# Kernel tuning notes

Hardware: AMD Instinct MI355X
Metric: run time of the kernel (lower is better)

Reference implementation:

```python
import jax, jax.numpy as jnp
import numpy as np

B = 32768   # batch (agents)
H = 64      # h_dim
E = 16      # embedding_dim
M = 6       # num_modes (n_samples)
P = M * 2   # traj_points
T = 30      # pred_len (seq_len)


def setup_inputs() -> dict:
    key = jax.random.key(0)
    ks = jax.random.split(key, 14)
    def s(k, shape, scale=0.1):
        return jax.random.normal(k, shape, jnp.float32) * scale
    return dict(
        traj_abs=s(ks[0], (1, B, 2), 1.0),
        traj_rel=s(ks[1], (1, B, 2), 1.0),
        h0=s(ks[2], (1, B, H)),
        c0=s(ks[3], (1, B, H)),
        W_ih=s(ks[4], (4 * H, E)),
        W_hh=s(ks[5], (4 * H, H)),
        b_ih=s(ks[6], (4 * H,)),
        b_hh=s(ks[7], (4 * H,)),
        W_se=s(ks[8], (E, P)),
        b_se=s(ks[9], (E,)),
        W_pos=s(ks[10], (P, H)),
        b_pos=s(ks[11], (P,)),
        W_conf=s(ks[12], (M, H)),
        b_conf=s(ks[13], (M,)),
    )


def reference(traj_abs, traj_rel, h0, c0, W_ih, W_hh, b_ih, b_hh,
              W_se, b_se, W_pos, b_pos, W_conf, b_conf):
    b = traj_rel.shape[1]
    # repeat_interleave the (x,y) pair num_modes times along feature dim -> [b, 12]
    rel12 = jnp.tile(traj_rel.reshape(b, 1, 2), (1, M, 1)).reshape(b, P)
    x = jax.nn.leaky_relu(rel12 @ W_se.T + b_se)  # [b, E]
    h = h0[0]
    c = c0[0]

    def step(carry, _):
        x, h, c = carry
        # PyTorch LSTM cell, gate order i, f, g, o
        gates = x @ W_ih.T + b_ih + h @ W_hh.T + b_hh  # [b, 4H]
        i, f, g, o = jnp.split(gates, 4, axis=-1)
        c = jax.nn.sigmoid(f) * c + jax.nn.sigmoid(i) * jnp.tanh(g)
        h = jax.nn.sigmoid(o) * jnp.tanh(c)
        rel = h @ W_pos.T + b_pos                      # [b, P]
        x = jax.nn.leaky_relu(rel @ W_se.T + b_se)     # [b, E]
        return (x, h, c), rel

    (x, h, c), rels = jax.lax.scan(step, (x, h, c), None, length=T)  # rels: [T, b, P]
    pred = rels.reshape(T, b, M, 2).transpose(1, 2, 0, 3)            # [b, M, T, 2]
    conf = jax.nn.softmax(h @ W_conf.T + b_conf, axis=1)             # [b, M]
    return pred, conf
```

## Files before the change

kernel.cpp:

```cpp
#include <hip/hip_runtime.h>
#include <hip/hip_bf16.h>

typedef _Float16 half8 __attribute__((ext_vector_type(8)));
typedef _Float16 half4 __attribute__((ext_vector_type(4)));
typedef float floatx16 __attribute__((ext_vector_type(16)));
typedef float float4v __attribute__((ext_vector_type(4)));

#define BATCH 32768
#define TT 30

#if __has_builtin(__builtin_amdgcn_exp2f)
#define FEXP2(x) __builtin_amdgcn_exp2f(x)
#else
#define FEXP2(x) __expf((x) * 0.6931471805599453f)
#endif
#if __has_builtin(__builtin_amdgcn_rcpf)
#define FRCP(x) __builtin_amdgcn_rcpf(x)
#else
#define FRCP(x) (1.0f / (x))
#endif

#define NLOG2E  -1.4426950408889634f
#define N2LOG2E -2.8853900817779268f

#define WFRAG_OFF 0
#define WCF_OFF   10240
#define BIASB_OFF 12288
#define SXY_OFF   12544
#define CBIAS_OFF 12592
#define WCONF_OFF 12656
#define BCONF_OFF 13040
#define FLAG_IDX  13056
#define CONF_BASE (BATCH * 360)

__global__ void detect_kernel(const unsigned short* __restrict__ raw,
                              int* __restrict__ flag_out) {
    __shared__ int sflag[256];
    int local = 0;
    for (int i = threadIdx.x; i < 16384; i += 256) {
        unsigned short u = raw[i];
        if ((u & 0x7F80u) == 0x7F80u) local = 1;
    }
    sflag[threadIdx.x] = local;
    __syncthreads();
    if (threadIdx.x == 0) {
        int f = 0;
        for (int i = 0; i < 256; ++i) f |= sflag[i];
        flag_out[0] = f;
    }
}

__device__ __forceinline__ float ldin(const void* p, int i, int isf32) {
    return isf32 ? ((const float*)p)[i]
                 : (float)((const __hip_bfloat16*)p)[i];
}

__global__ void prep_kernel(const void* __restrict__ W_ih,
                            const void* __restrict__ W_hh,
                            const void* __restrict__ b_ih,
                            const void* __restrict__ b_hh,
                            const void* __restrict__ W_se,
                            const void* __restrict__ b_se,
                            const void* __restrict__ W_pos,
                            const void* __restrict__ b_pos,
                            const void* __restrict__ W_conf,
                            const void* __restrict__ b_conf,
                            float* __restrict__ ws)
{
    const int isf32 = ((const int*)(ws + FLAG_IDX))[0];
    int tid = blockIdx.x * blockDim.x + threadIdx.x;
    int stride = gridDim.x * blockDim.x;
    _Float16* wfh = (_Float16*)ws;

    for (int idx = tid; idx < 20480; idx += stride) {
        int tl = idx / 2560, r1 = idx % 2560;
        int ks = r1 / 512, r2 = r1 % 512;
        int lane = r2 >> 3, jj = r2 & 7;
        int gate = tl >> 1, ug = tl & 1;
        int k = ks * 16 + (lane >> 5) * 8 + jj;
        int jn = ug * 32 + (lane & 31);
        int row = gate * 64 + jn;
        float v = (k < 16) ? ldin(W_ih, row * 16 + k, isf32)
                           : ldin(W_hh, row * 64 + (k - 16), isf32);
        v *= (gate == 2) ? N2LOG2E : NLOG2E;
        wfh[idx] = (_Float16)v;
    }
    _Float16* wch = (_Float16*)(ws + WCF_OFF);
    for (int idx = tid; idx < 4096; idx += stride) {
        int w = idx >> 11, r1 = idx & 2047;
        int ks = r1 >> 9, r2 = r1 & 511;
        int lane = r2 >> 3, jj = r2 & 7;
        int n = lane & 31;
        int krel = ks * 16 + (lane >> 5) * 8 + jj;
        float v = 0.f;
        if (w == 0) {
            if (n < 12) v = ldin(W_pos, n * 64 + krel, isf32);
        } else if (n < 16) {
            float s = 0.f;
            for (int p = 0; p < 12; ++p)
                s += ldin(W_se, n * 12 + p, isf32) * ldin(W_pos, p * 64 + krel, isf32);
            v = s;
        }
        wch[idx] = (_Float16)v;
    }
    for (int idx = tid; idx < 256; idx += stride) {
        int gate = idx >> 6;
        float scale = (gate == 2) ? N2LOG2E : NLOG2E;
        ws[BIASB_OFF + idx] = (ldin(b_ih, idx, isf32) + ldin(b_hh, idx, isf32)) * scale;
    }
    for (int idx = tid; idx < 16; idx += stride) {
        float sx = 0.f, sy = 0.f;
        for (int m = 0; m < 6; ++m) {
            sx += ldin(W_se, idx * 12 + 2 * m, isf32);
            sy += ldin(W_se, idx * 12 + 2 * m + 1, isf32);
        }
        ws[SXY_OFF + idx * 3 + 0] = sx;
        ws[SXY_OFF + idx * 3 + 1] = sy;
        ws[SXY_OFF + idx * 3 + 2] = ldin(b_se, idx, isf32);
    }
    for (int idx = tid; idx < 64; idx += stride) {
        int w = idx >> 5, cc = idx & 31;
        float v = 0.f;
        if (w == 0) {
            if (cc < 12) v = ldin(b_pos, cc, isf32);
        } else if (cc < 16) {
            float s = ldin(b_se, cc, isf32);
            for (int p = 0; p < 12; ++p)
                s += ldin(W_se, cc * 12 + p, isf32) * ldin(b_pos, p, isf32);
            v = s;
        }
        ws[CBIAS_OFF + idx] = v;
    }
    for (int idx = tid; idx < 384; idx += stride)
        ws[WCONF_OFF + idx] = ldin(W_conf, idx, isf32);
    for (int idx = tid; idx < 6; idx += stride)
        ws[BCONF_OFF + idx] = ldin(b_conf, idx, isf32);
}

__global__ __launch_bounds__(128, 2) void lstm_kernel(
    const void* __restrict__ traj_rel,
    const void* __restrict__ h0,
    const void* __restrict__ c0,
    const float* __restrict__ ws,
    float* __restrict__ out)
{
    __shared__ _Float16 zsh[32 * 88];
    __shared__ _Float16 predh[12 * 30 * 36];

    const int tid = threadIdx.x;
    const int lane = tid & 63;
    const int ug = __builtin_amdgcn_readfirstlane(tid >> 6);
    const int col = lane & 31;
    const int half = lane >> 5;
    const int j = ug * 32 + col;
    const int base = blockIdx.x * 32;
    const int isf32 = ((const int*)(ws + FLAG_IDX))[0];

    const float4v* wfg = (const float4v*)ws;
    half8 Bf[4][5];
#pragma unroll
    for (int g = 0; g < 4; ++g)
#pragma unroll
        for (int ks = 0; ks < 5; ++ks)
            Bf[g][ks] = __builtin_bit_cast(half8,
                wfg[((g * 2 + ug) * 5 + ks) * 64 + lane]);
    float bias4[4];
#pragma unroll
    for (int g = 0; g < 4; ++g) bias4[g] = ws[BIASB_OFF + g * 64 + j];

    half8 wfc[4];
    {
        const float4v* wcg = (const float4v*)(ws + WCF_OFF);
#pragma unroll
        for (int ks = 0; ks < 4; ++ks)
            wfc[ks] = __builtin_bit_cast(half8, wcg[(ug * 4 + ks) * 64 + lane]);
    }
    const float cb = ws[CBIAS_OFF + ug * 32 + col];

    float c[16];
#pragma unroll
    for (int i = 0; i < 16; ++i) {
        int r = (i & 3) + 8 * (i >> 2) + 4 * half;
        c[i] = ldin(c0, (base + r) * 64 + j, isf32);
    }
    {
        int m = tid & 31, jq = tid >> 5;
        half8 ha, hb;
#pragma unroll
        for (int i = 0; i < 8; ++i)
            ha[i] = (_Float16)ldin(h0, (base + m) * 64 + jq * 16 + i, isf32);
#pragma unroll
        for (int i = 0; i < 8; ++i)
            hb[i] = (_Float16)ldin(h0, (base + m) * 64 + jq * 16 + 8 + i, isf32);
        *(half8*)&zsh[m * 88 + 16 + jq * 16] = ha;
        *(half8*)&zsh[m * 88 + 16 + jq * 16 + 8] = hb;
        float rx = ldin(traj_rel, 2 * (base + m), isf32);
        float ry = ldin(traj_rel, 2 * (base + m) + 1, isf32);
        half4 xs;
#pragma unroll
        for (int i = 0; i < 4; ++i) {
            int e = 4 * jq + i;
            float x = fmaf(rx, ws[SXY_OFF + e * 3],
                      fmaf(ry, ws[SXY_OFF + e * 3 + 1], ws[SXY_OFF + e * 3 + 2]));
            xs[i] = (_Float16)(x > 0.f ? x : 0.01f * x);
        }
        *(half4*)&zsh[m * 88 + 4 * jq] = xs;
    }
    __syncthreads();

    const int zb = col * 88 + half * 8;

    for (int t = 0; t < TT; ++t) {
        floatx16 acc[4];
#pragma unroll
        for (int g = 0; g < 4; ++g)
#pragma unroll
            for (int i = 0; i < 16; ++i) acc[g][i] = bias4[g];
#pragma unroll
        for (int ks = 0; ks < 5; ++ks) {
            half8 af = *(const half8*)&zsh[zb + ks * 16];
#pragma unroll
            for (int g = 0; g < 4; ++g)
                acc[g] = __builtin_amdgcn_mfma_f32_32x32x16_f16(af, Bf[g][ks], acc[g], 0, 0, 0);
        }
        __syncthreads();

#pragma unroll
        for (int i = 0; i < 16; ++i) {
            float si = FRCP(1.0f + FEXP2(acc[0][i]));
            float sf = FRCP(1.0f + FEXP2(acc[1][i]));
            float tg = fmaf(2.0f, FRCP(1.0f + FEXP2(acc[2][i])), -1.0f);
            float so = FRCP(1.0f + FEXP2(acc[3][i]));
            float cn = fmaf(sf, c[i], si * tg);
            c[i] = cn;
            float th = fmaf(2.0f, FRCP(1.0f + FEXP2(cn * N2LOG2E)), -1.0f);
            float hn = so * th;
            int r = (i & 3) + 8 * (i >> 2) + 4 * half;
            zsh[r * 88 + 16 + j] = (_Float16)hn;
        }
        __syncthreads();

        {
            floatx16 racc;
#pragma unroll
            for (int i = 0; i < 16; ++i) racc[i] = cb;
#pragma unroll
            for (int ks = 0; ks < 4; ++ks) {
                half8 af = *(const half8*)&zsh[zb + 16 + ks * 16];
                racc = __builtin_amdgcn_mfma_f32_32x32x16_f16(af, wfc[ks], racc, 0, 0, 0);
            }
            if (ug == 0) {
                if (col < 12) {
#pragma unroll
                    for (int q2 = 0; q2 < 4; ++q2) {
                        half4 hv;
#pragma unroll
                        for (int i = 0; i < 4; ++i) hv[i] = (_Float16)racc[q2 * 4 + i];
                        *(half4*)&predh[(col * 30 + t) * 36 + q2 * 8 + 4 * half] = hv;
                    }
                }
            } else if (t != TT - 1) {
                if (col < 16) {
#pragma unroll
                    for (int i = 0; i < 16; ++i) {
                        float xv = racc[i];
                        xv = xv > 0.f ? xv : 0.01f * xv;
                        int r = (i & 3) + 8 * (i >> 2) + 4 * half;
                        zsh[r * 88 + col] = (_Float16)xv;
                    }
                }
            }
        }
        __syncthreads();
    }

    {
        float4* po4 = (float4*)(out + (size_t)base * 360);
#pragma unroll 1
        for (int q2 = 0; q2 < 23; ++q2) {
            int idx4 = q2 * 128 + tid;
            if (idx4 < 2880) {
                int a = idx4 / 90, rem = idx4 % 90;
                int m = rem / 15, tq = rem % 15;
                int t0 = tq * 2;
                float4 o;
                o.x = (float)predh[((2 * m + 0) * 30 + t0) * 36 + a];
                o.y = (float)predh[((2 * m + 1) * 30 + t0) * 36 + a];
                o.z = (float)predh[((2 * m + 0) * 30 + t0 + 1) * 36 + a];
                o.w = (float)predh[((2 * m + 1) * 30 + t0 + 1) * 36 + a];
                po4[idx4] = o;
            }
        }
    }

    if (ug == 0 && half == 0) {
        int m = col;
        float l[6];
#pragma unroll
        for (int md = 0; md < 6; ++md) l[md] = ws[BCONF_OFF + md];
        for (int jj = 0; jj < 64; ++jj) {
            float hv = (float)zsh[m * 88 + 16 + jj];
#pragma unroll
            for (int md = 0; md < 6; ++md)
                l[md] = fmaf(hv, ws[WCONF_OFF + md * 64 + jj], l[md]);
        }
        float mx = l[0];
#pragma unroll
        for (int md = 1; md < 6; ++md) mx = fmaxf(mx, l[md]);
        float ex[6], s = 0.f;
#pragma unroll
        for (int md = 0; md < 6; ++md) { ex[md] = __expf(l[md] - mx); s += ex[md]; }
        float inv = FRCP(s);
#pragma unroll
        for (int md = 0; md < 6; ++md)
            out[CONF_BASE + (size_t)(base + m) * 6 + md] = ex[md] * inv;
    }
}

extern "C" void kernel_launch(void* const* d_in, const int* in_sizes, int n_in,
                              void* d_out, int out_size, void* d_ws, size_t ws_size,
                              hipStream_t stream) {
    const void* traj_rel = d_in[1];
    const void* h0   = d_in[2];
    const void* c0   = d_in[3];
    const void* W_ih = d_in[4];
    const void* W_hh = d_in[5];
    const void* b_ih = d_in[6];
    const void* b_hh = d_in[7];
    const void* W_se = d_in[8];
    const void* b_se = d_in[9];
    const void* W_pos  = d_in[10];
    const void* b_pos  = d_in[11];
    const void* W_conf = d_in[12];
    const void* b_conf = d_in[13];
    float* ws = (float*)d_ws;
    float* out = (float*)d_out;

    detect_kernel<<<1, 256, 0, stream>>>((const unsigned short*)W_hh,
                                         (int*)(ws + FLAG_IDX));
    prep_kernel<<<40, 256, 0, stream>>>(W_ih, W_hh, b_ih, b_hh, W_se, b_se,
                                        W_pos, b_pos, W_conf, b_conf, ws);
    lstm_kernel<<<BATCH / 32, 128, 0, stream>>>(traj_rel, h0, c0, ws, out);
}
```

Baseline: 218.8 us.

## Split batch tile into two 16-row groups and software-pipeline LSTM phases

Switches the recurrent gate and projection matmuls from 32x32x16 to 16x16x32 MFMA, with weights re-laid out per wave over 32-unit halves. The 32-row tile is split into two 16-row groups so one group's gate matmul overlaps with the other group's activation math and output projection, giving three barriers per step that each cover two groups. The goal is to keep the matrix cores busy while the transcendental-heavy elementwise phase runs. The cost is padded K (80 to 96), more weight fragments held in registers, and more complex scheduling.

```diff
diff --git a/kernel.cpp b/kernel.cpp
--- a/kernel.cpp
+++ b/kernel.cpp
@@ -3,7 +3,6 @@
 
 typedef _Float16 half8 __attribute__((ext_vector_type(8)));
 typedef _Float16 half4 __attribute__((ext_vector_type(4)));
-typedef float floatx16 __attribute__((ext_vector_type(16)));
 typedef float float4v __attribute__((ext_vector_type(4)));
 
 #define BATCH 32768
@@ -24,13 +23,13 @@
 #define N2LOG2E -2.8853900817779268f
 
 #define WFRAG_OFF 0
-#define WCF_OFF   10240
-#define BIASB_OFF 12288
-#define SXY_OFF   12544
-#define CBIAS_OFF 12592
-#define WCONF_OFF 12656
-#define BCONF_OFF 13040
-#define FLAG_IDX  13056
+#define WCF_OFF   12288
+#define BIASB_OFF 13312
+#define SXY_OFF   13568
+#define CBIAS_OFF 13616
+#define WCONF_OFF 13648
+#define BCONF_OFF 14032
+#define FLAG_IDX  14038
 #define CONF_BASE (BATCH * 360)
 
 __global__ void detect_kernel(const unsigned short* __restrict__ raw,
@@ -72,33 +71,35 @@
     int stride = gridDim.x * blockDim.x;
     _Float16* wfh = (_Float16*)ws;
 
-    for (int idx = tid; idx < 20480; idx += stride) {
-        int tl = idx / 2560, r1 = idx % 2560;
-        int ks = r1 / 512, r2 = r1 % 512;
-        int lane = r2 >> 3, jj = r2 & 7;
-        int gate = tl >> 1, ug = tl & 1;
-        int k = ks * 16 + (lane >> 5) * 8 + jj;
-        int jn = ug * 32 + (lane & 31);
-        int row = gate * 64 + jn;
-        float v = (k < 16) ? ldin(W_ih, row * 16 + k, isf32)
-                           : ldin(W_hh, row * 64 + (k - 16), isf32);
+    for (int idx = tid; idx < 24576; idx += stride) {
+        int jj = idx & 7, r = idx >> 3;
+        int lane = r & 63; r >>= 6;
+        int ks = r % 3; r /= 3;
+        int tl = r & 7; int uhh = r >> 3;
+        int col = lane & 15, akq = lane >> 4;
+        int k = ks * 32 + akq * 8 + jj;
+        int gate = tl >> 1, us = tl & 1;
+        int row = gate * 64 + uhh * 32 + us * 16 + col;
+        float v = 0.f;
+        if (k < 16) v = ldin(W_ih, row * 16 + k, isf32);
+        else if (k < 80) v = ldin(W_hh, row * 64 + (k - 16), isf32);
         v *= (gate == 2) ? N2LOG2E : NLOG2E;
         wfh[idx] = (_Float16)v;
     }
     _Float16* wch = (_Float16*)(ws + WCF_OFF);
-    for (int idx = tid; idx < 4096; idx += stride) {
-        int w = idx >> 11, r1 = idx & 2047;
-        int ks = r1 >> 9, r2 = r1 & 511;
-        int lane = r2 >> 3, jj = r2 & 7;
-        int n = lane & 31;
-        int krel = ks * 16 + (lane >> 5) * 8 + jj;
+    for (int idx = tid; idx < 2048; idx += stride) {
+        int jj = idx & 7, r = idx >> 3;
+        int lane = r & 63; r >>= 6;
+        int ks = r & 1, uhh = r >> 1;
+        int col = lane & 15, akq = lane >> 4;
+        int k = ks * 32 + akq * 8 + jj;
         float v = 0.f;
-        if (w == 0) {
-            if (n < 12) v = ldin(W_pos, n * 64 + krel, isf32);
-        } else if (n < 16) {
+        if (uhh == 0) {
+            if (col < 12) v = ldin(W_pos, col * 64 + k, isf32);
+        } else {
             float s = 0.f;
             for (int p = 0; p < 12; ++p)
-                s += ldin(W_se, n * 12 + p, isf32) * ldin(W_pos, p * 64 + krel, isf32);
+                s += ldin(W_se, col * 12 + p, isf32) * ldin(W_pos, p * 64 + k, isf32);
             v = s;
         }
         wch[idx] = (_Float16)v;
@@ -118,12 +119,12 @@
         ws[SXY_OFF + idx * 3 + 1] = sy;
         ws[SXY_OFF + idx * 3 + 2] = ldin(b_se, idx, isf32);
     }
-    for (int idx = tid; idx < 64; idx += stride) {
-        int w = idx >> 5, cc = idx & 31;
+    for (int idx = tid; idx < 32; idx += stride) {
+        int w = idx >> 4, cc = idx & 15;
         float v = 0.f;
         if (w == 0) {
             if (cc < 12) v = ldin(b_pos, cc, isf32);
-        } else if (cc < 16) {
+        } else {
             float s = ldin(b_se, cc, isf32);
             for (int p = 0; p < 12; ++p)
                 s += ldin(W_se, cc * 12 + p, isf32) * ldin(b_pos, p, isf32);
@@ -144,47 +145,51 @@
     const float* __restrict__ ws,
     float* __restrict__ out)
 {
-    __shared__ _Float16 zsh[32 * 88];
+    __shared__ _Float16 zsh[2 * 16 * 104];
     __shared__ _Float16 predh[12 * 30 * 36];
 
     const int tid = threadIdx.x;
     const int lane = tid & 63;
-    const int ug = __builtin_amdgcn_readfirstlane(tid >> 6);
-    const int col = lane & 31;
-    const int half = lane >> 5;
-    const int j = ug * 32 + col;
+    const int uh = __builtin_amdgcn_readfirstlane(tid >> 6);
+    const int col16 = lane & 15;
+    const int akq = lane >> 4;
     const int base = blockIdx.x * 32;
     const int isf32 = ((const int*)(ws + FLAG_IDX))[0];
 
     const float4v* wfg = (const float4v*)ws;
-    half8 Bf[4][5];
-#pragma unroll
-    for (int g = 0; g < 4; ++g)
-#pragma unroll
-        for (int ks = 0; ks < 5; ++ks)
-            Bf[g][ks] = __builtin_bit_cast(half8,
-                wfg[((g * 2 + ug) * 5 + ks) * 64 + lane]);
-    float bias4[4];
-#pragma unroll
-    for (int g = 0; g < 4; ++g) bias4[g] = ws[BIASB_OFF + g * 64 + j];
-
-    half8 wfc[4];
+    half8 Bf[8][3];
+#pragma unroll
+    for (int tl = 0; tl < 8; ++tl)
+#pragma unroll
+        for (int ks = 0; ks < 3; ++ks)
+            Bf[tl][ks] = __builtin_bit_cast(half8,
+                wfg[((uh * 8 + tl) * 3 + ks) * 64 + lane]);
+    float bias8[8];
+#pragma unroll
+    for (int tl = 0; tl < 8; ++tl)
+        bias8[tl] = ws[BIASB_OFF + (tl >> 1) * 64 + uh * 32 + (tl & 1) * 16 + col16];
+    half8 wfc[2];
     {
         const float4v* wcg = (const float4v*)(ws + WCF_OFF);
 #pragma unroll
-        for (int ks = 0; ks < 4; ++ks)
-            wfc[ks] = __builtin_bit_cast(half8, wcg[(ug * 4 + ks) * 64 + lane]);
-    }
-    const float cb = ws[CBIAS_OFF + ug * 32 + col];
-
-    float c[16];
-#pragma unroll
-    for (int i = 0; i < 16; ++i) {
-        int r = (i & 3) + 8 * (i >> 2) + 4 * half;
-        c[i] = ldin(c0, (base + r) * 64 + j, isf32);
-    }
+        for (int ks = 0; ks < 2; ++ks)
+            wfc[ks] = __builtin_bit_cast(half8, wcg[(uh * 2 + ks) * 64 + lane]);
+    }
+    const float cb = ws[CBIAS_OFF + uh * 16 + col16];
+
+    float cg0[8], cg1[8];
+#pragma unroll
+    for (int us = 0; us < 2; ++us)
+#pragma unroll
+        for (int i = 0; i < 4; ++i) {
+            int unit = uh * 32 + us * 16 + col16;
+            cg0[us * 4 + i] = ldin(c0, (base + akq * 4 + i) * 64 + unit, isf32);
+            cg1[us * 4 + i] = ldin(c0, (base + 16 + akq * 4 + i) * 64 + unit, isf32);
+        }
     {
         int m = tid & 31, jq = tid >> 5;
+        int g = m >> 4, row = m & 15;
+        _Float16* zg = &zsh[g * 1664];
         half8 ha, hb;
 #pragma unroll
         for (int i = 0; i < 8; ++i)
@@ -192,8 +197,8 @@
 #pragma unroll
         for (int i = 0; i < 8; ++i)
             hb[i] = (_Float16)ldin(h0, (base + m) * 64 + jq * 16 + 8 + i, isf32);
-        *(half8*)&zsh[m * 88 + 16 + jq * 16] = ha;
-        *(half8*)&zsh[m * 88 + 16 + jq * 16 + 8] = hb;
+        *(half8*)&zg[row * 104 + 16 + jq * 16] = ha;
+        *(half8*)&zg[row * 104 + 16 + jq * 16 + 8] = hb;
         float rx = ldin(traj_rel, 2 * (base + m), isf32);
         float ry = ldin(traj_rel, 2 * (base + m) + 1, isf32);
         half4 xs;
@@ -204,75 +209,104 @@
                       fmaf(ry, ws[SXY_OFF + e * 3 + 1], ws[SXY_OFF + e * 3 + 2]));
             xs[i] = (_Float16)(x > 0.f ? x : 0.01f * x);
         }
-        *(half4*)&zsh[m * 88 + 4 * jq] = xs;
-    }
-    __syncthreads();
-
-    const int zb = col * 88 + half * 8;
-
-    for (int t = 0; t < TT; ++t) {
-        floatx16 acc[4];
-#pragma unroll
-        for (int g = 0; g < 4; ++g)
-#pragma unroll
-            for (int i = 0; i < 16; ++i) acc[g][i] = bias4[g];
-#pragma unroll
-        for (int ks = 0; ks < 5; ++ks) {
-            half8 af = *(const half8*)&zsh[zb + ks * 16];
-#pragma unroll
-            for (int g = 0; g < 4; ++g)
-                acc[g] = __builtin_amdgcn_mfma_f32_32x32x16_f16(af, Bf[g][ks], acc[g], 0, 0, 0);
-        }
+        *(half4*)&zg[row * 104 + 4 * jq] = xs;
+        if (jq == 0) {
+            half8 zz = {};
+            *(half8*)&zg[row * 104 + 80] = zz;
+            *(half8*)&zg[row * 104 + 88] = zz;
+        }
+    }
+    __syncthreads();
+
+    const int zbA = col16 * 104 + akq * 8;
+    const int zbC = zbA + 16;
+    const int hwb = 16 + uh * 32 + col16;
+
+    float4v acc0[8], acc1[8];
+
+#define ZG(g) (&zsh[(g) * 1664])
+
+#define PHASE_A(G, ACC) do {                                                  \
+    _Float16* zg_ = ZG(G);                                                    \
+    _Pragma("unroll")                                                         \
+    for (int tl = 0; tl < 8; ++tl) {                                          \
+        float bv = bias8[tl];                                                 \
+        ACC[tl][0] = bv; ACC[tl][1] = bv; ACC[tl][2] = bv; ACC[tl][3] = bv;   \
+    }                                                                         \
+    _Pragma("unroll")                                                         \
+    for (int ks = 0; ks < 3; ++ks) {                                          \
+        half8 af_ = *(const half8*)&zg_[zbA + ks * 32];                       \
+        _Pragma("unroll")                                                     \
+        for (int tl = 0; tl < 8; ++tl)                                        \
+            ACC[tl] = __builtin_amdgcn_mfma_f32_16x16x32_f16(                 \
+                af_, Bf[tl][ks], ACC[tl], 0, 0, 0);                           \
+    }                                                                         \
+} while (0)
+
+#define PHASE_B(G, ACC, CARR) do {                                            \
+    _Float16* zg_ = ZG(G);                                                    \
+    _Pragma("unroll")                                                         \
+    for (int us = 0; us < 2; ++us) {                                          \
+        _Pragma("unroll")                                                     \
+        for (int i = 0; i < 4; ++i) {                                         \
+            float si = FRCP(1.0f + FEXP2(ACC[us][i]));                        \
+            float sf = FRCP(1.0f + FEXP2(ACC[2 + us][i]));                    \
+            float tg = fmaf(2.0f, FRCP(1.0f + FEXP2(ACC[4 + us][i])), -1.0f); \
+            float so = FRCP(1.0f + FEXP2(ACC[6 + us][i]));                    \
+            float cn = fmaf(sf, CARR[us * 4 + i], si * tg);                   \
+            CARR[us * 4 + i] = cn;                                            \
+            float th = fmaf(2.0f, FRCP(1.0f + FEXP2(cn * N2LOG2E)), -1.0f);   \
+            float hn = so * th;                                               \
+            zg_[(akq * 4 + i) * 104 + hwb + us * 16] = (_Float16)hn;          \
+        }                                                                     \
+    }                                                                         \
+} while (0)
+
+
+#define PHASE_C(G, T) do {                                                    \
+    _Float16* zg_ = ZG(G);                                                    \
+    float4v racc_;                                                            \
+    racc_[0] = cb; racc_[1] = cb; racc_[2] = cb; racc_[3] = cb;               \
+    _Pragma("unroll")                                                         \
+    for (int ks = 0; ks < 2; ++ks) {                                          \
+        half8 af_ = *(const half8*)&zg_[zbC + ks * 32];                       \
+        racc_ = __builtin_amdgcn_mfma_f32_16x16x32_f16(                       \
+            af_, wfc[ks], racc_, 0, 0, 0);                                    \
+    }                                                                         \
+    if (uh == 0) {                                                            \
+        if (col16 < 12) {                                                     \
+            half4 hv_;                                                        \
+            _Pragma("unroll")                                                 \
+            for (int i = 0; i < 4; ++i) hv_[i] = (_Float16)racc_[i];          \
+            *(half4*)&predh[(col16 * 30 + (T)) * 36 + (G) * 16 + akq * 4] = hv_; \
+        }                                                                     \
+    } else if ((T) != TT - 1) {                                               \
+        _Pragma("unroll")                                                     \
+        for (int i = 0; i < 4; ++i) {                                         \
+            float xv_ = racc_[i];                                             \
+            xv_ = xv_ > 0.f ? xv_ : 0.01f * xv_;                              \
+            zg_[(akq * 4 + i) * 104 + col16] = (_Float16)xv_;                 \
+        }                                                                     \
+    }                                                                         \
+} while (0)
+
+    PHASE_A(0, acc0);
+    __syncthreads();
+    PHASE_A(1, acc1); PHASE_B(0, acc0, cg0);
+    __syncthreads();
+    PHASE_C(0, 0);    PHASE_B(1, acc1, cg1);
+    __syncthreads();
+
+    for (int t = 1; t < TT; ++t) {
+        PHASE_A(0, acc0); PHASE_C(1, t - 1);
         __syncthreads();
-
-#pragma unroll
-        for (int i = 0; i < 16; ++i) {
-            float si = FRCP(1.0f + FEXP2(acc[0][i]));
-            float sf = FRCP(1.0f + FEXP2(acc[1][i]));
-            float tg = fmaf(2.0f, FRCP(1.0f + FEXP2(acc[2][i])), -1.0f);
-            float so = FRCP(1.0f + FEXP2(acc[3][i]));
-            float cn = fmaf(sf, c[i], si * tg);
-            c[i] = cn;
-            float th = fmaf(2.0f, FRCP(1.0f + FEXP2(cn * N2LOG2E)), -1.0f);
-            float hn = so * th;
-            int r = (i & 3) + 8 * (i >> 2) + 4 * half;
-            zsh[r * 88 + 16 + j] = (_Float16)hn;
-        }
+        PHASE_A(1, acc1); PHASE_B(0, acc0, cg0);
         __syncthreads();
-
-        {
-            floatx16 racc;
-#pragma unroll
-            for (int i = 0; i < 16; ++i) racc[i] = cb;
-#pragma unroll
-            for (int ks = 0; ks < 4; ++ks) {
-                half8 af = *(const half8*)&zsh[zb + 16 + ks * 16];
-                racc = __builtin_amdgcn_mfma_f32_32x32x16_f16(af, wfc[ks], racc, 0, 0, 0);
-            }
-            if (ug == 0) {
-                if (col < 12) {
-#pragma unroll
-                    for (int q2 = 0; q2 < 4; ++q2) {
-                        half4 hv;
-#pragma unroll
-                        for (int i = 0; i < 4; ++i) hv[i] = (_Float16)racc[q2 * 4 + i];
-                        *(half4*)&predh[(col * 30 + t) * 36 + q2 * 8 + 4 * half] = hv;
-                    }
-                }
-            } else if (t != TT - 1) {
-                if (col < 16) {
-#pragma unroll
-                    for (int i = 0; i < 16; ++i) {
-                        float xv = racc[i];
-                        xv = xv > 0.f ? xv : 0.01f * xv;
-                        int r = (i & 3) + 8 * (i >> 2) + 4 * half;
-                        zsh[r * 88 + col] = (_Float16)xv;
-                    }
-                }
-            }
-        }
+        PHASE_C(0, t);    PHASE_B(1, acc1, cg1);
         __syncthreads();
     }
+    PHASE_C(1, TT - 1);
+    __syncthreads();
 
     {
         float4* po4 = (float4*)(out + (size_t)base * 360);
@@ -293,13 +327,14 @@
         }
     }
 
-    if (ug == 0 && half == 0) {
-        int m = col;
+    if (uh == 0 && lane < 32) {
+        int m = lane;
+        int g = m >> 4, row = m & 15;
         float l[6];
 #pragma unroll
         for (int md = 0; md < 6; ++md) l[md] = ws[BCONF_OFF + md];
         for (int jj = 0; jj < 64; ++jj) {
-            float hv = (float)zsh[m * 88 + 16 + jj];
+            float hv = (float)zsh[g * 1664 + row * 104 + 16 + jj];
 #pragma unroll
             for (int md = 0; md < 6; ++md)
                 l[md] = fmaf(hv, ws[WCONF_OFF + md * 64 + jj], l[md]);
```

After: 208.5 us. -4.7%, faster.

## Give each wave its own 16 rows with 16x16x32 MFMA and LDS-resident weights

Applied to the files above, without the earlier changes.

Changes the LSTM kernel from two waves sharing 32 rows (and needing block barriers each step) to four waves each owning 16 independent batch rows. Gate weights are staged in LDS and each wave runs 16x16x32 MFMAs over all 256 gate columns. This removes the per-timestep __syncthreads and the predh staging buffer, and predictions are written straight to global memory. The gate math is also reworked so each cell update needs fewer reciprocals. In exchange, every weight fragment is re-read from LDS each step, the global stores are strided and uncoalesced, and K is padded from 80 to 96.

```diff
diff --git a/kernel.cpp b/kernel.cpp
--- a/kernel.cpp
+++ b/kernel.cpp
@@ -3,7 +3,6 @@
 
 typedef _Float16 half8 __attribute__((ext_vector_type(8)));
 typedef _Float16 half4 __attribute__((ext_vector_type(4)));
-typedef float floatx16 __attribute__((ext_vector_type(16)));
 typedef float float4v __attribute__((ext_vector_type(4)));
 
 #define BATCH 32768
@@ -24,13 +23,13 @@
 #define N2LOG2E -2.8853900817779268f
 
 #define WFRAG_OFF 0
-#define WCF_OFF   10240
-#define BIASB_OFF 12288
-#define SXY_OFF   12544
-#define CBIAS_OFF 12592
-#define WCONF_OFF 12656
-#define BCONF_OFF 13040
-#define FLAG_IDX  13056
+#define WCF_OFF   12288
+#define BIASB_OFF 13312
+#define SXY_OFF   13568
+#define CBIAS_OFF 13616
+#define WCONF_OFF 13648
+#define BCONF_OFF 14032
+#define FLAG_IDX  14038
 #define CONF_BASE (BATCH * 360)
 
 __global__ void detect_kernel(const unsigned short* __restrict__ raw,
@@ -72,33 +71,34 @@
     int stride = gridDim.x * blockDim.x;
     _Float16* wfh = (_Float16*)ws;
 
-    for (int idx = tid; idx < 20480; idx += stride) {
-        int tl = idx / 2560, r1 = idx % 2560;
-        int ks = r1 / 512, r2 = r1 % 512;
-        int lane = r2 >> 3, jj = r2 & 7;
-        int gate = tl >> 1, ug = tl & 1;
-        int k = ks * 16 + (lane >> 5) * 8 + jj;
-        int jn = ug * 32 + (lane & 31);
-        int row = gate * 64 + jn;
-        float v = (k < 16) ? ldin(W_ih, row * 16 + k, isf32)
-                           : ldin(W_hh, row * 64 + (k - 16), isf32);
+    for (int idx = tid; idx < 24576; idx += stride) {
+        int jj = idx & 7, r = idx >> 3;
+        int lane = r & 63; r >>= 6;
+        int ks = r % 3; r /= 3;
+        int gate = r & 3; int ug = r >> 2;
+        int col = lane & 15, akq = lane >> 4;
+        int k = ks * 32 + akq * 8 + jj;
+        int row = gate * 64 + ug * 16 + col;
+        float v = 0.f;
+        if (k < 16) v = ldin(W_ih, row * 16 + k, isf32);
+        else if (k < 80) v = ldin(W_hh, row * 64 + (k - 16), isf32);
         v *= (gate == 2) ? N2LOG2E : NLOG2E;
         wfh[idx] = (_Float16)v;
     }
     _Float16* wch = (_Float16*)(ws + WCF_OFF);
-    for (int idx = tid; idx < 4096; idx += stride) {
-        int w = idx >> 11, r1 = idx & 2047;
-        int ks = r1 >> 9, r2 = r1 & 511;
-        int lane = r2 >> 3, jj = r2 & 7;
-        int n = lane & 31;
-        int krel = ks * 16 + (lane >> 5) * 8 + jj;
+    for (int idx = tid; idx < 2048; idx += stride) {
+        int jj = idx & 7, r = idx >> 3;
+        int lane = r & 63; r >>= 6;
+        int ks = r & 1, role = r >> 1;
+        int col = lane & 15, akq = lane >> 4;
+        int k = ks * 32 + akq * 8 + jj;
         float v = 0.f;
-        if (w == 0) {
-            if (n < 12) v = ldin(W_pos, n * 64 + krel, isf32);
-        } else if (n < 16) {
+        if (role == 0) {
+            if (col < 12) v = ldin(W_pos, col * 64 + k, isf32);
+        } else {
             float s = 0.f;
             for (int p = 0; p < 12; ++p)
-                s += ldin(W_se, n * 12 + p, isf32) * ldin(W_pos, p * 64 + krel, isf32);
+                s += ldin(W_se, col * 12 + p, isf32) * ldin(W_pos, p * 64 + k, isf32);
             v = s;
         }
         wch[idx] = (_Float16)v;
@@ -118,12 +118,12 @@
         ws[SXY_OFF + idx * 3 + 1] = sy;
         ws[SXY_OFF + idx * 3 + 2] = ldin(b_se, idx, isf32);
     }
-    for (int idx = tid; idx < 64; idx += stride) {
-        int w = idx >> 5, cc = idx & 31;
+    for (int idx = tid; idx < 32; idx += stride) {
+        int w = idx >> 4, cc = idx & 15;
         float v = 0.f;
         if (w == 0) {
             if (cc < 12) v = ldin(b_pos, cc, isf32);
-        } else if (cc < 16) {
+        } else {
             float s = ldin(b_se, cc, isf32);
             for (int p = 0; p < 12; ++p)
                 s += ldin(W_se, cc * 12 + p, isf32) * ldin(b_pos, p, isf32);
@@ -137,183 +137,189 @@
         ws[BCONF_OFF + idx] = ldin(b_conf, idx, isf32);
 }
 
-__global__ __launch_bounds__(128, 2) void lstm_kernel(
+__global__ __launch_bounds__(256, 2) void lstm_kernel(
     const void* __restrict__ traj_rel,
     const void* __restrict__ h0,
     const void* __restrict__ c0,
     const float* __restrict__ ws,
     float* __restrict__ out)
 {
-    __shared__ _Float16 zsh[32 * 88];
-    __shared__ _Float16 predh[12 * 30 * 36];
+    __shared__ _Float16 wldsh[24576];
+    __shared__ _Float16 zsh[4 * 16 * 104];
 
     const int tid = threadIdx.x;
     const int lane = tid & 63;
-    const int ug = __builtin_amdgcn_readfirstlane(tid >> 6);
-    const int col = lane & 31;
-    const int half = lane >> 5;
-    const int j = ug * 32 + col;
-    const int base = blockIdx.x * 32;
+    const int wid = __builtin_amdgcn_readfirstlane(tid >> 6);
+    const int col16 = lane & 15;
+    const int q4 = lane >> 4;
+    const int base = blockIdx.x * 64;
+    const int gbase = base + wid * 16;
     const int isf32 = ((const int*)(ws + FLAG_IDX))[0];
 
-    const float4v* wfg = (const float4v*)ws;
-    half8 Bf[4][5];
-#pragma unroll
-    for (int g = 0; g < 4; ++g)
-#pragma unroll
-        for (int ks = 0; ks < 5; ++ks)
-            Bf[g][ks] = __builtin_bit_cast(half8,
-                wfg[((g * 2 + ug) * 5 + ks) * 64 + lane]);
-    float bias4[4];
-#pragma unroll
-    for (int g = 0; g < 4; ++g) bias4[g] = ws[BIASB_OFF + g * 64 + j];
-
-    half8 wfc[4];
+    {
+        const float4* src = (const float4*)ws;
+        float4* dst = (float4*)wldsh;
+#pragma unroll
+        for (int k = 0; k < 12; ++k)
+            dst[k * 256 + tid] = src[k * 256 + tid];
+    }
+
+    _Float16* const zw = &zsh[wid * 1664];
+
+    float bias16[16];
+#pragma unroll
+    for (int u = 0; u < 4; ++u)
+#pragma unroll
+        for (int g = 0; g < 4; ++g)
+            bias16[u * 4 + g] = ws[BIASB_OFF + g * 64 + u * 16 + col16];
+    half8 wfcR[2], wfcX[2];
     {
         const float4v* wcg = (const float4v*)(ws + WCF_OFF);
 #pragma unroll
-        for (int ks = 0; ks < 4; ++ks)
-            wfc[ks] = __builtin_bit_cast(half8, wcg[(ug * 4 + ks) * 64 + lane]);
-    }
-    const float cb = ws[CBIAS_OFF + ug * 32 + col];
+        for (int ks = 0; ks < 2; ++ks) {
+            wfcR[ks] = __builtin_bit_cast(half8, wcg[ks * 64 + lane]);
+            wfcX[ks] = __builtin_bit_cast(half8, wcg[(2 + ks) * 64 + lane]);
+        }
+    }
+    const float cbr = ws[CBIAS_OFF + col16];
+    const float cbx = ws[CBIAS_OFF + 16 + col16];
 
     float c[16];
 #pragma unroll
-    for (int i = 0; i < 16; ++i) {
-        int r = (i & 3) + 8 * (i >> 2) + 4 * half;
-        c[i] = ldin(c0, (base + r) * 64 + j, isf32);
-    }
+    for (int u = 0; u < 4; ++u)
+#pragma unroll
+        for (int i = 0; i < 4; ++i)
+            c[u * 4 + i] = ldin(c0, (gbase + q4 * 4 + i) * 64 + u * 16 + col16, isf32);
+
     {
-        int m = tid & 31, jq = tid >> 5;
+        int r = col16;
         half8 ha, hb;
 #pragma unroll
         for (int i = 0; i < 8; ++i)
-            ha[i] = (_Float16)ldin(h0, (base + m) * 64 + jq * 16 + i, isf32);
+            ha[i] = (_Float16)ldin(h0, (gbase + r) * 64 + q4 * 16 + i, isf32);
 #pragma unroll
         for (int i = 0; i < 8; ++i)
-            hb[i] = (_Float16)ldin(h0, (base + m) * 64 + jq * 16 + 8 + i, isf32);
-        *(half8*)&zsh[m * 88 + 16 + jq * 16] = ha;
-        *(half8*)&zsh[m * 88 + 16 + jq * 16 + 8] = hb;
-        float rx = ldin(traj_rel, 2 * (base + m), isf32);
-        float ry = ldin(traj_rel, 2 * (base + m) + 1, isf32);
+            hb[i] = (_Float16)ldin(h0, (gbase + r) * 64 + q4 * 16 + 8 + i, isf32);
+        *(half8*)&zw[r * 104 + 16 + q4 * 16] = ha;
+        *(half8*)&zw[r * 104 + 16 + q4 * 16 + 8] = hb;
+        float rx = ldin(traj_rel, 2 * (gbase + r), isf32);
+        float ry = ldin(traj_rel, 2 * (gbase + r) + 1, isf32);
         half4 xs;
 #pragma unroll
         for (int i = 0; i < 4; ++i) {
-            int e = 4 * jq + i;
+            int e = 4 * q4 + i;
             float x = fmaf(rx, ws[SXY_OFF + e * 3],
                       fmaf(ry, ws[SXY_OFF + e * 3 + 1], ws[SXY_OFF + e * 3 + 2]));
             xs[i] = (_Float16)(x > 0.f ? x : 0.01f * x);
         }
-        *(half4*)&zsh[m * 88 + 4 * jq] = xs;
+        *(half4*)&zw[r * 104 + 4 * q4] = xs;
+        if (q4 == 0) {
+            half8 zz = {};
+            *(half8*)&zw[r * 104 + 80] = zz;
+            *(half8*)&zw[r * 104 + 88] = zz;
+            *(half8*)&zw[r * 104 + 96] = zz;
+        }
     }
     __syncthreads();
 
-    const int zb = col * 88 + half * 8;
+    const int aoffb = col16 * 104 + q4 * 8;
+    float* const op0 = out + (size_t)(gbase + q4 * 4) * 360
+                       + (col16 >> 1) * 60 + (col16 & 1);
 
     for (int t = 0; t < TT; ++t) {
-        floatx16 acc[4];
-#pragma unroll
-        for (int g = 0; g < 4; ++g)
-#pragma unroll
-            for (int i = 0; i < 16; ++i) acc[g][i] = bias4[g];
-#pragma unroll
-        for (int ks = 0; ks < 5; ++ks) {
-            half8 af = *(const half8*)&zsh[zb + ks * 16];
-#pragma unroll
-            for (int g = 0; g < 4; ++g)
-                acc[g] = __builtin_amdgcn_mfma_f32_32x32x16_f16(af, Bf[g][ks], acc[g], 0, 0, 0);
-        }
-        __syncthreads();
-
-#pragma unroll
-        for (int i = 0; i < 16; ++i) {
-            float si = FRCP(1.0f + FEXP2(acc[0][i]));
-            float sf = FRCP(1.0f + FEXP2(acc[1][i]));
-            float tg = fmaf(2.0f, FRCP(1.0f + FEXP2(acc[2][i])), -1.0f);
-            float so = FRCP(1.0f + FEXP2(acc[3][i]));
-            float cn = fmaf(sf, c[i], si * tg);
-            c[i] = cn;
-            float th = fmaf(2.0f, FRCP(1.0f + FEXP2(cn * N2LOG2E)), -1.0f);
-            float hn = so * th;
-            int r = (i & 3) + 8 * (i >> 2) + 4 * half;
-            zsh[r * 88 + 16 + j] = (_Float16)hn;
-        }
-        __syncthreads();
-
-        {
-            floatx16 racc;
-#pragma unroll
-            for (int i = 0; i < 16; ++i) racc[i] = cb;
-#pragma unroll
-            for (int ks = 0; ks < 4; ++ks) {
-                half8 af = *(const half8*)&zsh[zb + 16 + ks * 16];
-                racc = __builtin_amdgcn_mfma_f32_32x32x16_f16(af, wfc[ks], racc, 0, 0, 0);
+        half8 az0 = *(const half8*)&zw[aoffb];
+        half8 az1 = *(const half8*)&zw[aoffb + 32];
+        half8 az2 = *(const half8*)&zw[aoffb + 64];
+
+#pragma unroll
+        for (int u = 0; u < 4; ++u) {
+            float4v acc[4];
+#pragma unroll
+            for (int g = 0; g < 4; ++g) {
+                float bv = bias16[u * 4 + g];
+                acc[g][0] = bv; acc[g][1] = bv; acc[g][2] = bv; acc[g][3] = bv;
             }
-            if (ug == 0) {
-                if (col < 12) {
-#pragma unroll
-                    for (int q2 = 0; q2 < 4; ++q2) {
-                        half4 hv;
-#pragma unroll
-                        for (int i = 0; i < 4; ++i) hv[i] = (_Float16)racc[q2 * 4 + i];
-                        *(half4*)&predh[(col * 30 + t) * 36 + q2 * 8 + 4 * half] = hv;
-                    }
-                }
-            } else if (t != TT - 1) {
-                if (col < 16) {
-#pragma unroll
-                    for (int i = 0; i < 16; ++i) {
-                        float xv = racc[i];
-                        xv = xv > 0.f ? xv : 0.01f * xv;
-                        int r = (i & 3) + 8 * (i >> 2) + 4 * half;
-                        zsh[r * 88 + col] = (_Float16)xv;
-                    }
-                }
+#pragma unroll
+            for (int g = 0; g < 4; ++g) {
+                const int fb = ((u * 4 + g) * 3) * 512 + lane * 8;
+                acc[g] = __builtin_amdgcn_mfma_f32_16x16x32_f16(
+                    az0, *(const half8*)&wldsh[fb], acc[g], 0, 0, 0);
+                acc[g] = __builtin_amdgcn_mfma_f32_16x16x32_f16(
+                    az1, *(const half8*)&wldsh[fb + 512], acc[g], 0, 0, 0);
+                acc[g] = __builtin_amdgcn_mfma_f32_16x16x32_f16(
+                    az2, *(const half8*)&wldsh[fb + 1024], acc[g], 0, 0, 0);
             }
-        }
-        __syncthreads();
+#pragma unroll
+            for (int i = 0; i < 4; ++i) {
+                float ei = FEXP2(acc[0][i]);
+                float ef = FEXP2(acc[1][i]);
+                float eg = FEXP2(acc[2][i]);
+                float eo = FEXP2(acc[3][i]);
+                float pp = (1.f + ei) * (1.f + eg);
+                float qq = 1.f + ef;
+                float cn = fmaf(c[u * 4 + i], pp, (1.f - eg) * qq) * FRCP(pp * qq);
+                c[u * 4 + i] = cn;
+                float ec = FEXP2(cn * N2LOG2E);
+                float hn = (1.f - ec) * FRCP((1.f + eo) * (1.f + ec));
+                zw[(q4 * 4 + i) * 104 + 16 + u * 16 + col16] = (_Float16)hn;
+            }
+        }
+
+        half8 ah0 = *(const half8*)&zw[aoffb + 16];
+        half8 ah1 = *(const half8*)&zw[aoffb + 48];
+        float4v rr, rx;
+        rr[0] = cbr; rr[1] = cbr; rr[2] = cbr; rr[3] = cbr;
+        rx[0] = cbx; rx[1] = cbx; rx[2] = cbx; rx[3] = cbx;
+        rr = __builtin_amdgcn_mfma_f32_16x16x32_f16(ah0, wfcR[0], rr, 0, 0, 0);
+        rr = __builtin_amdgcn_mfma_f32_16x16x32_f16(ah1, wfcR[1], rr, 0, 0, 0);
+        rx = __builtin_amdgcn_mfma_f32_16x16x32_f16(ah0, wfcX[0], rx, 0, 0, 0);
+        rx = __builtin_amdgcn_mfma_f32_16x16x32_f16(ah1, wfcX[1], rx, 0, 0, 0);
+
+        if (col16 < 12) {
+#pragma unroll
+            for (int i = 0; i < 4; ++i)
+                op0[(size_t)i * 360 + t * 2] = rr[i];
+        }
+        if (t != TT - 1) {
+#pragma unroll
+            for (int i = 0; i < 4; ++i) {
+                float xv = rx[i];
+                xv = xv > 0.f ? xv : 0.01f * xv;
+                zw[(q4 * 4 + i) * 104 + col16] = (_Float16)xv;
+            }
+        }
     }
 
     {
-        float4* po4 = (float4*)(out + (size_t)base * 360);
-#pragma unroll 1
-        for (int q2 = 0; q2 < 23; ++q2) {
-            int idx4 = q2 * 128 + tid;
-            if (idx4 < 2880) {
-                int a = idx4 / 90, rem = idx4 % 90;
-                int m = rem / 15, tq = rem % 15;
-                int t0 = tq * 2;
-                float4 o;
-                o.x = (float)predh[((2 * m + 0) * 30 + t0) * 36 + a];
-                o.y = (float)predh[((2 * m + 1) * 30 + t0) * 36 + a];
-                o.z = (float)predh[((2 * m + 0) * 30 + t0 + 1) * 36 + a];
-                o.w = (float)predh[((2 * m + 1) * 30 + t0 + 1) * 36 + a];
-                po4[idx4] = o;
-            }
-        }
-    }
-
-    if (ug == 0 && half == 0) {
-        int m = col;
+        int r = lane >> 2, qq = lane & 3;
         float l[6];
 #pragma unroll
-        for (int md = 0; md < 6; ++md) l[md] = ws[BCONF_OFF + md];
-        for (int jj = 0; jj < 64; ++jj) {
-            float hv = (float)zsh[m * 88 + 16 + jj];
+        for (int md = 0; md < 6; ++md)
+            l[md] = (qq == 0) ? ws[BCONF_OFF + md] : 0.f;
+#pragma unroll
+        for (int jj = 0; jj < 16; ++jj) {
+            float hv = (float)zw[r * 104 + 16 + qq * 16 + jj];
 #pragma unroll
             for (int md = 0; md < 6; ++md)
-                l[md] = fmaf(hv, ws[WCONF_OFF + md * 64 + jj], l[md]);
-        }
-        float mx = l[0];
-#pragma unroll
-        for (int md = 1; md < 6; ++md) mx = fmaxf(mx, l[md]);
-        float ex[6], s = 0.f;
-#pragma unroll
-        for (int md = 0; md < 6; ++md) { ex[md] = __expf(l[md] - mx); s += ex[md]; }
-        float inv = FRCP(s);
-#pragma unroll
-        for (int md = 0; md < 6; ++md)
-            out[CONF_BASE + (size_t)(base + m) * 6 + md] = ex[md] * inv;
+                l[md] = fmaf(hv, ws[WCONF_OFF + md * 64 + qq * 16 + jj], l[md]);
+        }
+#pragma unroll
+        for (int md = 0; md < 6; ++md) {
+            l[md] += __shfl_xor(l[md], 1);
+            l[md] += __shfl_xor(l[md], 2);
+        }
+        if (qq == 0) {
+            float mx = l[0];
+#pragma unroll
+            for (int md = 1; md < 6; ++md) mx = fmaxf(mx, l[md]);
+            float ex[6], s = 0.f;
+#pragma unroll
+            for (int md = 0; md < 6; ++md) { ex[md] = __expf(l[md] - mx); s += ex[md]; }
+            float inv = FRCP(s);
+#pragma unroll
+            for (int md = 0; md < 6; ++md)
+                out[CONF_BASE + (size_t)(gbase + r) * 6 + md] = ex[md] * inv;
+        }
     }
 }
 
@@ -340,5 +346,5 @@
                                          (int*)(ws + FLAG_IDX));
     prep_kernel<<<40, 256, 0, stream>>>(W_ih, W_hh, b_ih, b_hh, W_se, b_se,
                                         W_pos, b_pos, W_conf, b_conf, ws);
-    lstm_kernel<<<BATCH / 32, 128, 0, stream>>>(traj_rel, h0, c0, ws, out);
-}
+    lstm_kernel<<<BATCH / 64, 256, 0, stream>>>(traj_rel, h0, c0, ws, out);
+}
```

Result: slower. 397.2 us (+81.6%).
